# Optimization experiments

Measured on AMD Instinct MI355X. Metric: run time of the kernel, lower is better.

The kernel has to match this reference:

```python
import jax, jax.numpy as jnp
import numpy as np

_MAX_SQRT_GRADIENT = 1000.0

@jax.custom_vjp
def sqrt_bound(x):
    return jnp.sqrt(x)

def _sb_fwd(x):
    return jnp.sqrt(x), x

def _sb_bwd(x, g):
    return (g / jnp.sqrt(jnp.maximum(4.0 * x, 1.0 / (_MAX_SQRT_GRADIENT ** 2))),)

sqrt_bound.defvjp(_sb_fwd, _sb_bwd)


def setup_inputs() -> dict:
    B, S, H, L, NH, K = 2, 4096, 2048, 2048, 16, 4
    BW = L // NH
    key = jax.random.key(0)
    ks = jax.random.split(key, 8)
    f = lambda k, shape: jax.random.normal(k, shape, dtype=jnp.float32) * 0.02
    return {
        "input_states": jax.random.normal(ks[0], (B, S, H), dtype=jnp.float32),
        "Wy": f(ks[1], (H, L)), "by": jnp.zeros((L,), jnp.float32),
        "Wx": f(ks[2], (H, L)), "bx": jnp.zeros((L,), jnp.float32),
        "conv_w": f(ks[3], (L, 1, K)), "conv_b": jnp.zeros((L,), jnp.float32),
        "rec_param": f(ks[4], (L,)),
        "igw": f(ks[5], (NH, BW, BW)), "igb": jnp.zeros((NH, BW), jnp.float32),
        "rgw": f(ks[6], (NH, BW, BW)), "rgb": jnp.zeros((NH, BW), jnp.float32),
        "Wout": f(ks[7], (L, H)), "bout": jnp.zeros((H,), jnp.float32),
        "position_ids": jnp.tile(jnp.arange(S, dtype=jnp.int32), (B, 1)),
    }


def reference(input_states, Wy, by, Wx, bx, conv_w, conv_b, rec_param,
              igw, igb, rgw, rgb, Wout, bout, position_ids):
    B, S, H = input_states.shape
    L = Wy.shape[1]
    NH, BW = igw.shape[0], igw.shape[1]
    K = conv_w.shape[-1]

    # y branch: linear + gelu
    y = jax.nn.gelu(input_states @ Wy + by)                      # [B,S,L]

    # x branch: linear + causal depthwise conv1d
    x = input_states @ Wx + bx                                    # [B,S,L]
    xc = jnp.transpose(x, (0, 2, 1))                              # [B,L,S]
    xc = jax.lax.conv_general_dilated(
        xc, conv_w, window_strides=(1,), padding=[(K - 1, 0)],
        dimension_numbers=("NCH", "OIH", "NCH"), feature_group_count=L)
    x = jnp.transpose(xc, (0, 2, 1)) + conv_b                     # [B,S,L]

    # RG-LRU block-diagonal gates
    xh = x.reshape(B, S, NH, BW)
    ig = jax.nn.sigmoid(jnp.einsum("bsnd,nde->bsne", xh, igw) + igb).reshape(B, S, L)
    rg = jax.nn.sigmoid(jnp.einsum("bsnd,nde->bsne", xh, rgw) + rgb).reshape(B, S, L)

    log_a = -8.0 * rg * jax.nn.softplus(rec_param)                # [B,S,L]
    a = jnp.exp(log_a)
    reset = (position_ids == 0)[:, :, None]                       # [B,S,1]

    mult = sqrt_bound(1.0 - jnp.exp(2.0 * log_a))
    mult = jnp.where(reset, 1.0, mult)
    normed = x * ig * mult                                        # [B,S,L]
    a_eff = jnp.where(reset, 0.0, a)                              # [B,S,L]

    def step(h, inp):
        a_t, x_t = inp
        h = a_t.astype(jnp.float32) * h + x_t.astype(jnp.float32)
        return h, h

    h0 = jnp.zeros((B, L), jnp.float32)
    _, hs = jax.lax.scan(step, h0,
                         (jnp.swapaxes(a_eff, 0, 1), jnp.swapaxes(normed, 0, 1)))
    hs = jnp.swapaxes(hs, 0, 1).astype(input_states.dtype)        # [B,S,L]

    return (hs * y) @ Wout + bout                                 # [B,S,H]
```

## Files before the change

kernel.cpp:

```cpp
#include <hip/hip_runtime.h>
#include <cstdint>
#include <cstddef>

#define B_  2
#define S_  4096
#define H_  2048
#define L_  2048
#define NH_ 16
#define M_  (B_*S_)
#define NC_ 64
#define CS_ 64

typedef unsigned short u16;
typedef short  bf8v  __attribute__((ext_vector_type(8)));
typedef u16    u16x8 __attribute__((ext_vector_type(8)));
typedef float  f32x4 __attribute__((ext_vector_type(4)));

__device__ __forceinline__ float bf2f(u16 u){
  union { unsigned i; float f; } v; v.i = ((unsigned)u) << 16; return v.f;
}
__device__ __forceinline__ u16 f2bf(float f){
  union { float f; unsigned i; } v; v.f = f;
  unsigned u = v.i;
  return (u16)((u + 0x7FFFu + ((u >> 16) & 1u)) >> 16);
}
__device__ __forceinline__ float bfr(float f){ return bf2f(f2bf(f)); }
__device__ __forceinline__ void gld16(const void* g, void* l){
  __builtin_amdgcn_global_load_lds((const __attribute__((address_space(1))) void*)g,
                                   (__attribute__((address_space(3))) void*)l, 16, 0, 0);
}

__global__ __launch_bounds__(256)
void gemm_bf16(const u16* __restrict__ A, int lda,
               const u16* __restrict__ Bt, int K,
               const float* __restrict__ bias1, const float* __restrict__ bias2,
               void* __restrict__ C1, u16* __restrict__ C2, int ldc,
               int gelu_flag, int f32out)
{
  __shared__ u16 Alds[128*64];
  __shared__ u16 Blds[128*64];
  const int t    = threadIdx.x;
  const int lane = t & 63;
  const int w    = t >> 6;
  const int wr   = w >> 1, wc = w & 1;
  const int lr   = lane & 15, lk = lane >> 4;

  const int nwg = gridDim.x * gridDim.y;
  const int bid = blockIdx.y * gridDim.x + blockIdx.x;
  const int cpx = nwg >> 3;
  const int swz = (bid & 7) * cpx + (bid >> 3);
  const int bx  = swz % gridDim.x;
  const int by  = swz / gridDim.x;

  const long rowA0 = (long)by * 128;
  const long colB0 = (long)bx * 128;
  const u16* Ag = A  + rowA0 * lda;
  const u16* Bg = Bt + colB0 * K;
  const int srow = t >> 3, scol = t & 7;

#define STAGE(KT) do {                                                     \
    _Pragma("unroll")                                                      \
    for (int it = 0; it < 4; ++it) {                                       \
      int r  = it*32 + srow;                                               \
      int ca = (scol ^ (r & 7)) * 8;                                       \
      gld16(Ag + (long)r*lda + (long)(KT)*64 + ca, Alds + it*2048 + t*8);  \
      gld16(Bg + (long)r*K   + (long)(KT)*64 + ca, Blds + it*2048 + t*8);  \
    } } while(0)

  f32x4 acc[4][4];
#pragma unroll
  for (int m=0;m<4;m++)
#pragma unroll
    for (int n=0;n<4;n++) acc[m][n] = (f32x4){0.f,0.f,0.f,0.f};

  const int nk = K / 64;
  STAGE(0);
  __syncthreads();

  for (int kt = 0; kt < nk; ++kt) {
    bf8v af[4][2], bv[4][2];
#pragma unroll
    for (int m=0;m<4;m++)
#pragma unroll
      for (int ks=0;ks<2;ks++){
        int r  = wr*64 + m*16 + lr;
        int kb = (ks*32 + lk*8)*2;
        af[m][ks] = *(const bf8v*)((const char*)Alds + r*128 + (kb ^ ((r&7)<<4)));
      }
#pragma unroll
    for (int n=0;n<4;n++)
#pragma unroll
      for (int ks=0;ks<2;ks++){
        int r  = wc*64 + n*16 + lr;
        int kb = (ks*32 + lk*8)*2;
        bv[n][ks] = *(const bf8v*)((const char*)Blds + r*128 + (kb ^ ((r&7)<<4)));
      }
    __syncthreads();
    if (kt + 1 < nk) STAGE(kt + 1);
    __builtin_amdgcn_sched_barrier(0);
#pragma unroll
    for (int ks=0;ks<2;ks++)
#pragma unroll
      for (int m=0;m<4;m++)
#pragma unroll
        for (int n=0;n<4;n++)
          acc[m][n] = __builtin_amdgcn_mfma_f32_16x16x32_bf16(af[m][ks], bv[n][ks], acc[m][n], 0, 0, 0);
    if (kt + 1 < nk) __syncthreads();
  }
#undef STAGE

  u16*   Cb = (u16*)C1;
  float* Cf = (float*)C1;
#pragma unroll
  for (int m=0;m<4;m++){
    long row = rowA0 + wr*64 + m*16 + lk*4;
#pragma unroll
    for (int n=0;n<4;n++){
      int col = (int)colB0 + wc*64 + n*16 + lr;
      bool sec = (C2 != nullptr) && (col >= L_);
      float bvv = sec ? bias2[col - L_] : bias1[col];
      bool gel = gelu_flag && !sec;
#pragma unroll
      for (int rr=0; rr<4; ++rr){
        float v = acc[m][n][rr] + bvv;
        if (gel) {
          float u  = 0.7978845608028654f * (v + 0.044715f * v*v*v);
          float tu = fminf(fmaxf(2.f*u, -80.f), 80.f);
          float e  = __expf(tu);
          float th = (e - 1.f) / (e + 1.f);
          v = 0.5f * v * (1.f + th);
        }
        if (sec)          C2[(row+rr)*(long)L_ + (col - L_)] = f2bf(v);
        else if (f32out)  Cf[(row+rr)*(long)ldc + col] = v;
        else              Cb[(row+rr)*(long)ldc + col] = f2bf(v);
      }
    }
  }
}

__global__ __launch_bounds__(256)
void gates_fused(const u16* __restrict__ Xlin, const float* __restrict__ cw,
                 const float* __restrict__ cb, const u16* __restrict__ Gt,
                 const float* __restrict__ gbias, const float* __restrict__ c8,
                 const int* __restrict__ pos,
                 u16* __restrict__ Ae, u16* __restrict__ Nr,
                 float* __restrict__ Ach, float* __restrict__ Hch)
{
  __shared__ __align__(16) char sm[16384 + 32768];
  const int t  = threadIdx.x;
  const int sc = blockIdx.x;
  const int n  = blockIdx.y;
  const int b  = blockIdx.z;
  const int s0 = sc*64;
  const long rowg0 = (long)b*S_ + s0;

  char* xc = sm;
  u16*  xs = (u16*)(sm + 16384);
  char* bs = sm + 16384;

  for (int it=0; it<5; ++it){
    int slot = it*256 + t;
    if (slot < 67*16){
      int i = slot >> 4, c = slot & 15;
      int s = s0 - 3 + i;
      u16x8 v = (u16x8){0,0,0,0,0,0,0,0};
      if (s >= 0)
        v = *(const u16x8*)(Xlin + ((long)b*S_ + s)*L_ + n*128 + c*8);
      *(u16x8*)(xs + i*128 + c*8) = v;
    }
  }
  __syncthreads();

#pragma unroll
  for (int it=0; it<4; ++it){
    int slot = it*256 + t;
    int row = slot >> 4, c = slot & 15;
    int d0 = c*8;
    float a8[8];
#pragma unroll
    for (int j=0;j<8;j++) a8[j] = cb[n*128 + d0 + j];
#pragma unroll
    for (int k=0;k<4;k++){
      u16x8 xv = *(const u16x8*)(xs + (row+k)*128 + d0);
#pragma unroll
      for (int j=0;j<8;j++)
        a8[j] += bf2f(xv[j]) * cw[(n*128 + d0 + j)*4 + k];
    }
    u16x8 o;
#pragma unroll
    for (int j=0;j<8;j++) o[j] = f2bf(a8[j]);
    *(u16x8*)(xc + row*256 + ((d0*2) ^ ((row&7)<<4))) = o;
  }
  __syncthreads();

  const int w  = t >> 6;
  const int lane = t & 63;
  const int lr = lane & 15, lk = lane >> 4;
  const int arow = w*16 + lr;

  bf8v af[4];
#pragma unroll
  for (int ks=0;ks<4;ks++)
    af[ks] = *(const bf8v*)(xc + arow*256 + ((ks*64 + lk*16) ^ ((arow&7)<<4)));

  f32x4 aig[8], brg[8];
#pragma unroll
  for (int half=0; half<2; ++half){
#pragma unroll
    for (int it=0; it<8; ++it){
      int slot = it*256 + t;
      int jr = slot >> 4, c = slot & 15;
      gld16(Gt + (size_t)(n*256 + half*128 + jr)*128 + (size_t)((c ^ (jr&7))*8),
            bs + slot*16);
    }
    __syncthreads();
#pragma unroll
    for (int nf=0; nf<8; ++nf){
      f32x4 acc = (f32x4){0.f,0.f,0.f,0.f};
      int jrow = nf*16 + lr;
#pragma unroll
      for (int ks=0;ks<4;ks++){
        bf8v bv = *(const bf8v*)(bs + jrow*256 + ((ks*64 + lk*16) ^ ((jrow&7)<<4)));
        acc = __builtin_amdgcn_mfma_f32_16x16x32_bf16(af[ks], bv, acc, 0, 0, 0);
      }
      if (half==0) aig[nf] = acc; else brg[nf] = acc;
    }
    __syncthreads();
  }

  float* wsA = (float*)bs;
  float* wsh = (float*)(bs + 2048);
  bool rst[4];
#pragma unroll
  for (int rr=0; rr<4; ++rr) rst[rr] = (pos[rowg0 + w*16 + lk*4 + rr] == 0);

#pragma unroll
  for (int nf=0; nf<8; ++nf){
    int dl = nf*16 + lr;
    float gb1 = gbias[n*256 + dl];
    float gb2 = gbias[n*256 + 128 + dl];
    float cc8 = c8[n*128 + dl];
    float Aseg = 1.f, hseg = 0.f;
#pragma unroll
    for (int rr=0; rr<4; ++rr){
      int row = w*16 + lk*4 + rr;
      long gs = rowg0 + row;
      float ig = 1.f / (1.f + __expf(-(aig[nf][rr] + gb1)));
      float rg = 1.f / (1.f + __expf(-(brg[nf][rr] + gb2)));
      float la = cc8 * rg;
      float a  = __expf(la);
      float mult = rst[rr] ? 1.f : sqrtf(fmaxf(1.f - __expf(2.f*la), 0.f));
      u16 xv = *(const u16*)(xc + row*256 + ((dl*2) ^ ((row&7)<<4)));
      float x = bf2f(xv);
      float nrv = bfr(x * ig * mult);
      float aev = rst[rr] ? 0.f : bfr(a);
      Nr[gs*L_ + n*128 + dl] = f2bf(nrv);
      Ae[gs*L_ + n*128 + dl] = f2bf(aev);
      hseg = fmaf(aev, hseg, nrv);
      Aseg *= aev;
    }
    {
      float Ap = __shfl_xor(Aseg, 16);
      float hp = __shfl_xor(hseg, 16);
      bool low = ((lk & 1) == 0);
      float Alo = low ? Aseg : Ap, Ahi = low ? Ap : Aseg;
      float hlo = low ? hseg : hp, hhi = low ? hp : hseg;
      Aseg = Alo * Ahi; hseg = fmaf(Ahi, hlo, hhi);
      Ap = __shfl_xor(Aseg, 32);
      hp = __shfl_xor(hseg, 32);
      low = ((lk & 2) == 0);
      Alo = low ? Aseg : Ap; Ahi = low ? Ap : Aseg;
      hlo = low ? hseg : hp; hhi = low ? hp : hseg;
      Aseg = Alo * Ahi; hseg = fmaf(Ahi, hlo, hhi);
    }
    if (lk == 0){ wsA[w*128 + dl] = Aseg; wsh[w*128 + dl] = hseg; }
  }
  __syncthreads();
  if (t < 128){
    float A = wsA[t], h = wsh[t];
#pragma unroll
    for (int ww=1; ww<4; ++ww){
      float Aw = wsA[ww*128 + t], hw = wsh[ww*128 + t];
      h = fmaf(Aw, h, hw);
      A *= Aw;
    }
    long o = ((long)b*NC_ + sc)*L_ + n*128 + t;
    Ach[o] = A; Hch[o] = h;
  }
}

__global__ __launch_bounds__(256)
void prep_all(const float* __restrict__ Wy, const float* __restrict__ Wx,
              const float* __restrict__ Wout,
              u16* __restrict__ WyT, u16* __restrict__ WxT, u16* __restrict__ WoT,
              const float* __restrict__ igw, const float* __restrict__ rgw,
              const float* __restrict__ igb, const float* __restrict__ rgb,
              const float* __restrict__ rec, u16* __restrict__ Gt,
              float* __restrict__ gbias, float* __restrict__ c8,
              const float* __restrict__ X, u16* __restrict__ Xb)
{
  const int bidg = blockIdx.x;
  const int t = threadIdx.x;
  if (bidg < 3072) {
    int z   = bidg >> 10;
    int rem = bidg & 1023;
    const float* in  = (z == 0) ? Wy  : (z == 1) ? Wx  : Wout;
    u16*         out = (z == 0) ? WyT : (z == 1) ? WxT : WoT;
    const int R = 2048, C = 2048;
    __shared__ float tile[64][65];
    int tc = (rem & 31) * 64, tr = (rem >> 5) * 64;
    int r  = t >> 2, c0 = (t & 3) * 16;
#pragma unroll
    for (int i=0;i<4;i++)
      *(f32x4*)(&tile[r][c0 + i*4]) = *(const f32x4*)(in + (long)(tr+r)*C + tc + c0 + i*4);
    __syncthreads();
    int nl = t >> 2;
#pragma unroll
    for (int it=0; it<2; ++it){
      int g = (t & 3) + it*4;
      u16x8 o;
#pragma unroll
      for (int e=0;e<8;e++) o[e] = f2bf(tile[g*8+e][nl]);
      *(u16x8*)(out + (long)(tc+nl)*R + tr + g*8) = o;
    }
  } else if (bidg < 5120) {
    int idx = (bidg - 3072)*256 + t;
    int d = idx & 127, g = idx >> 7;
    int n = g >> 8, j = g & 255;
    float v = (j < 128) ? igw[(n*128 + d)*128 + j] : rgw[(n*128 + d)*128 + (j-128)];
    Gt[idx] = f2bf(v);
    if (idx < NH_*256) {
      int nn = idx >> 8, jj = idx & 255;
      gbias[idx] = (jj < 128) ? igb[nn*128 + jj] : rgb[nn*128 + jj - 128];
    }
    if (idx < L_) c8[idx] = -8.f * log1pf(__expf(rec[idx]));
  } else {
    long idx = (long)(bidg - 5120)*256 + t;
    f32x4 a = *(const f32x4*)(X + idx*8);
    f32x4 b = *(const f32x4*)(X + idx*8 + 4);
    u16x8 o;
#pragma unroll
    for (int e=0;e<4;e++){ o[e] = f2bf(a[e]); o[4+e] = f2bf(b[e]); }
    *(u16x8*)(Xb + idx*8) = o;
  }
}

__global__ __launch_bounds__(256)
void scan3(const u16* __restrict__ Ae, const u16* __restrict__ Nr,
           const float* __restrict__ Ach, const float* __restrict__ Hch,
           const u16* __restrict__ Y, u16* __restrict__ Z)
{
  int t = threadIdx.x;
  int l = (blockIdx.x & 7)*256 + t;
  int c = (NC_-1) - ((blockIdx.x >> 3) & (NC_-1));
  int b = blockIdx.x >> 9;
  float h = 0.f;
#pragma unroll 4
  for (int cc = 0; cc < c; ++cc){
    long o = ((long)b*NC_ + cc)*L_ + l;
    h = fmaf(Ach[o], h, Hch[o]);
  }
  long base = ((long)b*S_ + (long)c*CS_)*L_ + l;
#pragma unroll 8
  for (int s=0; s<CS_; ++s){
    long o = base + (long)s*L_;
    h = fmaf(bf2f(Ae[o]), h, bf2f(Nr[o]));
    Z[o] = f2bf(h * bf2f(Y[o]));
  }
}

extern "C" void kernel_launch(void* const* d_in, const int* in_sizes, int n_in,
                              void* d_out, int out_size, void* d_ws, size_t ws_size,
                              hipStream_t stream)
{
  (void)in_sizes; (void)n_in; (void)out_size; (void)ws_size;
  const float* X    = (const float*)d_in[0];
  const float* Wy   = (const float*)d_in[1];
  const float* by   = (const float*)d_in[2];
  const float* Wx   = (const float*)d_in[3];
  const float* bx   = (const float*)d_in[4];
  const float* cw   = (const float*)d_in[5];
  const float* cb   = (const float*)d_in[6];
  const float* rec  = (const float*)d_in[7];
  const float* igw  = (const float*)d_in[8];
  const float* igb  = (const float*)d_in[9];
  const float* rgw  = (const float*)d_in[10];
  const float* rgb  = (const float*)d_in[11];
  const float* Wout = (const float*)d_in[12];
  const float* bout = (const float*)d_in[13];
  const int*   pos  = (const int*)d_in[14];
  float* out = (float*)d_out;

  char* ws = (char*)d_ws;
  size_t o_Xbf  = 0;
  size_t o_Xlin = o_Xbf  + (size_t)M_*H_*2;
  size_t o_WyT  = o_Xlin + (size_t)M_*L_*2;
  size_t o_WxT  = o_WyT  + (size_t)H_*L_*2;
  size_t o_WoT  = o_WxT  + (size_t)H_*L_*2;
  size_t o_Gt   = o_WoT  + (size_t)L_*H_*2;
  size_t o_gb   = o_Gt   + (size_t)NH_*256*128*2;
  size_t o_c8   = o_gb   + 4096*4;
  size_t o_Y    = o_c8   + 2048*4;
  size_t o_xc   = o_Y    + (size_t)M_*L_*2;
  size_t o_Ae   = o_xc   + (size_t)M_*L_*2;
  size_t o_Nr   = o_Ae   + (size_t)M_*L_*2;
  size_t o_Ach  = o_Nr   + (size_t)M_*L_*2;
  size_t o_Hch  = o_Ach  + (size_t)B_*NC_*L_*4;

  u16*   Xbf   = (u16*)(ws + o_Xbf);
  u16*   Xlin  = (u16*)(ws + o_Xlin);
  u16*   WyT   = (u16*)(ws + o_WyT);
  u16*   WxT   = (u16*)(ws + o_WxT);
  u16*   WoT   = (u16*)(ws + o_WoT);
  u16*   Gt    = (u16*)(ws + o_Gt);
  float* gbias = (float*)(ws + o_gb);
  float* c8    = (float*)(ws + o_c8);
  u16*   Y     = (u16*)(ws + o_Y);
  u16*   Z     = (u16*)(ws + o_xc);
  u16*   Ae    = (u16*)(ws + o_Ae);
  u16*   Nr    = (u16*)(ws + o_Nr);
  float* Ach   = (float*)(ws + o_Ach);
  float* Hch   = (float*)(ws + o_Hch);

  dim3 blk(256);
  prep_all<<<dim3(13312), blk, 0, stream>>>(Wy, Wx, Wout, WyT, WxT, WoT,
                                            igw, rgw, igb, rgb, rec, Gt, gbias, c8,
                                            X, Xbf);
  gemm_bf16<<<dim3(32,64), blk, 0, stream>>>(Xbf, H_, WyT, H_, by, bx, Y, Xlin, L_, 1, 0);
  gates_fused<<<dim3(NC_, NH_, B_), blk, 0, stream>>>(Xlin, cw, cb, Gt, gbias, c8, pos,
                                                      Ae, Nr, Ach, Hch);
  scan3<<<dim3(1024), blk, 0, stream>>>(Ae, Nr, Ach, Hch, Y, Z);
  gemm_bf16<<<dim3(16,64), blk, 0, stream>>>(Z, L_, WoT, L_, bout, bout, out, nullptr, H_, 0, 1);
}
```

Baseline: 412.6 us.

## Replace GEMM with 256x256 tile, 8-wave, double-buffered ping-pong pipelined kernel

Replaces the 128x128 single-buffered bf16 GEMM with a 256x256-tile, 512-thread kernel. It uses double-buffered LDS (128KB), inline-asm ds_read_b128 with immediate offsets, and explicit waitcnt and barrier phases so that global-to-LDS loads and LDS reads overlap MFMA work. s_setprio is raised around the MFMA blocks. The larger tile increases data reuse per LDS byte, at the cost of fewer workgroups (512 and 256 blocks) and higher register and LDS pressure, which may hurt occupancy. Tile wraparound with modulo loads redundant tiles in the last iterations.

```diff
diff --git a/kernel.cpp b/kernel.cpp
--- a/kernel.cpp
+++ b/kernel.cpp
@@ -29,20 +29,99 @@
   __builtin_amdgcn_global_load_lds((const __attribute__((address_space(1))) void*)g,
                                    (__attribute__((address_space(3))) void*)l, 16, 0, 0);
 }
-
-__global__ __launch_bounds__(256)
-void gemm_bf16(const u16* __restrict__ A, int lda,
-               const u16* __restrict__ Bt, int K,
-               const float* __restrict__ bias1, const float* __restrict__ bias2,
-               void* __restrict__ C1, u16* __restrict__ C2, int ldc,
-               int gelu_flag, int f32out)
+__device__ __forceinline__ unsigned ldsoff(const void* p){
+  return (unsigned)(uintptr_t)(const __attribute__((address_space(3))) void*)p;
+}
+template<int IMM>
+__device__ __forceinline__ bf8v dsr(unsigned addr){
+  bf8v r;
+  asm volatile("ds_read_b128 %0, %1 offset:%c2" : "=v"(r) : "v"(addr), "i"(IMM));
+  return r;
+}
+
+#define SB0_()     __builtin_amdgcn_sched_barrier(0)
+#define BARRIER_() do{ __builtin_amdgcn_s_barrier(); SB0_(); }while(0)
+#define LGKM0_()   do{ asm volatile("s_waitcnt lgkmcnt(0)" ::: "memory"); SB0_(); }while(0)
+#define VMC8_()    do{ asm volatile("s_waitcnt vmcnt(8)" ::: "memory"); SB0_(); }while(0)
+
+struct StageCtx { const u16* sA; const u16* sB; int lda; int K; char* ldsc; unsigned dst; };
+
+__device__ __forceinline__ void stgA(const StageCtx& c, int buf, int h, int tile){
+#pragma unroll
+  for (int r=0;r<2;r++){
+    int rr = h*128 + r*64;
+    gld16(c.sA + (size_t)rr*c.lda + (size_t)tile*64, c.ldsc + buf*32768 + c.dst + rr*128);
+  }
+}
+__device__ __forceinline__ void stgB(const StageCtx& c, int buf, int h, int tile){
+#pragma unroll
+  for (int r=0;r<2;r++){
+    int rr = h*128 + r*64;
+    gld16(c.sB + (size_t)rr*c.K + (size_t)tile*64, c.ldsc + 65536 + buf*32768 + c.dst + rr*128);
+  }
+}
+
+#define MFMAQ(ARR, MH, NHH) do{                                                 \
+  __builtin_amdgcn_s_setprio(1);                                                \
+  _Pragma("unroll") for (int ks=0;ks<2;ks++)                                    \
+  _Pragma("unroll") for (int dm=0;dm<4;dm++)                                    \
+  _Pragma("unroll") for (int dn=0;dn<2;dn++)                                    \
+    acc[(MH)*4+dm][(NHH)*2+dn] = __builtin_amdgcn_mfma_f32_16x16x32_bf16(       \
+        ARR[dm][ks], b[(NHH)*2+dn][ks], acc[(MH)*4+dm][(NHH)*2+dn], 0,0,0);     \
+  __builtin_amdgcn_s_setprio(0);                                                \
+}while(0)
+
+template<int D>
+__device__ __forceinline__ void tile_phase(
+    bf8v (&a)[4][2], bf8v (&aN)[4][2], bf8v (&b)[4][2], f32x4 (&acc)[8][4],
+    unsigned aA0, unsigned aA1, unsigned aB0, unsigned aB1,
+    const StageCtx& ctx, int tp2)
 {
-  __shared__ u16 Alds[128*64];
-  __shared__ u16 Blds[128*64];
+  constexpr int DB = D*32768;
+  constexpr int OB = (1-D)*32768;
+  b[2][0]=dsr<DB+4096>(aB0); b[2][1]=dsr<DB+4096>(aB1);
+  b[3][0]=dsr<DB+6144>(aB0); b[3][1]=dsr<DB+6144>(aB1);
+  SB0_();
+  MFMAQ(a, 0, 0);
+  LGKM0_(); BARRIER_();
+  aN[0][0]=dsr<DB+ 8192>(aA0); aN[0][1]=dsr<DB+ 8192>(aA1);
+  aN[1][0]=dsr<DB+10240>(aA0); aN[1][1]=dsr<DB+10240>(aA1);
+  aN[2][0]=dsr<DB+12288>(aA0); aN[2][1]=dsr<DB+12288>(aA1);
+  aN[3][0]=dsr<DB+14336>(aA0); aN[3][1]=dsr<DB+14336>(aA1);
+  SB0_();
+  MFMAQ(a, 0, 1);
+  LGKM0_(); BARRIER_();
+  stgB(ctx, D, 0, tp2);
+  SB0_();
+  MFMAQ(aN, 1, 0);
+  SB0_();
+  stgB(ctx, D, 1, tp2);
+  stgA(ctx, D, 0, tp2);
+  stgA(ctx, D, 1, tp2);
+  VMC8_();
+  a[0][0]=dsr<OB+   0>(aA0); a[0][1]=dsr<OB+   0>(aA1);
+  a[1][0]=dsr<OB+2048>(aA0); a[1][1]=dsr<OB+2048>(aA1);
+  a[2][0]=dsr<OB+4096>(aA0); a[2][1]=dsr<OB+4096>(aA1);
+  a[3][0]=dsr<OB+6144>(aA0); a[3][1]=dsr<OB+6144>(aA1);
+  b[0][0]=dsr<OB+   0>(aB0); b[0][1]=dsr<OB+   0>(aB1);
+  b[1][0]=dsr<OB+2048>(aB0); b[1][1]=dsr<OB+2048>(aB1);
+  SB0_();
+  MFMAQ(aN, 1, 1);
+  LGKM0_(); BARRIER_();
+}
+
+__global__ __launch_bounds__(512)
+void gemm256p(const u16* __restrict__ A, int lda,
+              const u16* __restrict__ Bt, int K,
+              const float* __restrict__ bias1, const float* __restrict__ bias2,
+              void* __restrict__ C1, u16* __restrict__ C2, int ldc,
+              int gelu_flag, int f32out)
+{
+  __shared__ __align__(16) u16 lds[65536];
   const int t    = threadIdx.x;
   const int lane = t & 63;
   const int w    = t >> 6;
-  const int wr   = w >> 1, wc = w & 1;
+  const int wm   = w >> 2, wn = w & 3;
   const int lr   = lane & 15, lk = lane >> 4;
 
   const int nwg = gridDim.x * gridDim.y;
@@ -52,77 +131,69 @@
   const int bx  = swz % gridDim.x;
   const int by  = swz / gridDim.x;
 
-  const long rowA0 = (long)by * 128;
-  const long colB0 = (long)bx * 128;
+  const long rowA0 = (long)by * 256;
+  const long colB0 = (long)bx * 256;
   const u16* Ag = A  + rowA0 * lda;
   const u16* Bg = Bt + colB0 * K;
-  const int srow = t >> 3, scol = t & 7;
-
-#define STAGE(KT) do {                                                     \
-    _Pragma("unroll")                                                      \
-    for (int it = 0; it < 4; ++it) {                                       \
-      int r  = it*32 + srow;                                               \
-      int ca = (scol ^ (r & 7)) * 8;                                       \
-      gld16(Ag + (long)r*lda + (long)(KT)*64 + ca, Alds + it*2048 + t*8);  \
-      gld16(Bg + (long)r*K   + (long)(KT)*64 + ca, Blds + it*2048 + t*8);  \
-    } } while(0)
-
-  f32x4 acc[4][4];
-#pragma unroll
-  for (int m=0;m<4;m++)
+
+  char* ldsc = (char*)lds;
+  StageCtx ctx;
+  ctx.sA  = Ag + (size_t)(t>>3)*lda + ((t&7) ^ ((t>>3)&7))*8;
+  ctx.sB  = Bg + (size_t)(t>>3)*K   + ((t&7) ^ ((t>>3)&7))*8;
+  ctx.lda = lda; ctx.K = K; ctx.ldsc = ldsc;
+  ctx.dst = (unsigned)((t>>3)*128 + (t&7)*16);
+
+  const unsigned lb  = ldsoff(lds);
+  const unsigned swx = (unsigned)((lr & 7) << 4);
+  const unsigned aA0 = lb + (wm*128 + lr)*128 + ((      lk*16) ^ swx);
+  const unsigned aA1 = lb + (wm*128 + lr)*128 + ((64 +  lk*16) ^ swx);
+  const unsigned aB0 = lb + 65536 + (wn*64 + lr)*128 + ((      lk*16) ^ swx);
+  const unsigned aB1 = lb + 65536 + (wn*64 + lr)*128 + ((64 +  lk*16) ^ swx);
+
+  f32x4 acc[8][4];
+#pragma unroll
+  for (int m=0;m<8;m++)
 #pragma unroll
     for (int n=0;n<4;n++) acc[m][n] = (f32x4){0.f,0.f,0.f,0.f};
-
-  const int nk = K / 64;
-  STAGE(0);
-  __syncthreads();
-
-  for (int kt = 0; kt < nk; ++kt) {
-    bf8v af[4][2], bv[4][2];
-#pragma unroll
-    for (int m=0;m<4;m++)
-#pragma unroll
-      for (int ks=0;ks<2;ks++){
-        int r  = wr*64 + m*16 + lr;
-        int kb = (ks*32 + lk*8)*2;
-        af[m][ks] = *(const bf8v*)((const char*)Alds + r*128 + (kb ^ ((r&7)<<4)));
-      }
-#pragma unroll
-    for (int n=0;n<4;n++)
-#pragma unroll
-      for (int ks=0;ks<2;ks++){
-        int r  = wc*64 + n*16 + lr;
-        int kb = (ks*32 + lk*8)*2;
-        bv[n][ks] = *(const bf8v*)((const char*)Blds + r*128 + (kb ^ ((r&7)<<4)));
-      }
-    __syncthreads();
-    if (kt + 1 < nk) STAGE(kt + 1);
-    __builtin_amdgcn_sched_barrier(0);
-#pragma unroll
-    for (int ks=0;ks<2;ks++)
-#pragma unroll
-      for (int m=0;m<4;m++)
-#pragma unroll
-        for (int n=0;n<4;n++)
-          acc[m][n] = __builtin_amdgcn_mfma_f32_16x16x32_bf16(af[m][ks], bv[n][ks], acc[m][n], 0, 0, 0);
-    if (kt + 1 < nk) __syncthreads();
-  }
-#undef STAGE
+  bf8v a[4][2], aN[4][2], b[4][2];
+
+  const int nkt = K / 64;
+  stgB(ctx, 0, 0, 0);        stgB(ctx, 0, 1, 0);
+  stgA(ctx, 0, 0, 0);        stgA(ctx, 0, 1, 0);
+  stgB(ctx, 1, 0, 1 % nkt);  stgB(ctx, 1, 1, 1 % nkt);
+  stgA(ctx, 1, 0, 1 % nkt);  stgA(ctx, 1, 1, 1 % nkt);
+  VMC8_();
+  BARRIER_();
+  a[0][0]=dsr<   0>(aA0); a[0][1]=dsr<   0>(aA1);
+  a[1][0]=dsr<2048>(aA0); a[1][1]=dsr<2048>(aA1);
+  a[2][0]=dsr<4096>(aA0); a[2][1]=dsr<4096>(aA1);
+  a[3][0]=dsr<6144>(aA0); a[3][1]=dsr<6144>(aA1);
+  b[0][0]=dsr<   0>(aB0); b[0][1]=dsr<   0>(aB1);
+  b[1][0]=dsr<2048>(aB0); b[1][1]=dsr<2048>(aB1);
+  LGKM0_();
+
+  for (int i = 0; i < nkt/2; ++i) {
+    int t0 = 2*i;
+    tile_phase<0>(a, aN, b, acc, aA0, aA1, aB0, aB1, ctx, (t0+2)%nkt);
+    tile_phase<1>(a, aN, b, acc, aA0, aA1, aB0, aB1, ctx, (t0+3)%nkt);
+  }
 
   u16*   Cb = (u16*)C1;
   float* Cf = (float*)C1;
-#pragma unroll
-  for (int m=0;m<4;m++){
-    long row = rowA0 + wr*64 + m*16 + lk*4;
-#pragma unroll
-    for (int n=0;n<4;n++){
-      int col = (int)colB0 + wc*64 + n*16 + lr;
+  const long rowW = rowA0 + wm*128;
+  const int  colW = (int)colB0 + wn*64;
+#pragma unroll
+  for (int mf=0;mf<8;mf++){
+    long row = rowW + mf*16 + lk*4;
+#pragma unroll
+    for (int nf=0;nf<4;nf++){
+      int col = colW + nf*16 + lr;
       bool sec = (C2 != nullptr) && (col >= L_);
       float bvv = sec ? bias2[col - L_] : bias1[col];
       bool gel = gelu_flag && !sec;
 #pragma unroll
       for (int rr=0; rr<4; ++rr){
-        float v = acc[m][n][rr] + bvv;
+        float v = acc[mf][nf][rr] + bvv;
         if (gel) {
           float u  = 0.7978845608028654f * (v + 0.044715f * v*v*v);
           float tu = fminf(fmaxf(2.f*u, -80.f), 80.f);
@@ -426,9 +497,9 @@
   prep_all<<<dim3(13312), blk, 0, stream>>>(Wy, Wx, Wout, WyT, WxT, WoT,
                                             igw, rgw, igb, rgb, rec, Gt, gbias, c8,
                                             X, Xbf);
-  gemm_bf16<<<dim3(32,64), blk, 0, stream>>>(Xbf, H_, WyT, H_, by, bx, Y, Xlin, L_, 1, 0);
+  gemm256p<<<dim3(16,32), dim3(512), 0, stream>>>(Xbf, H_, WyT, H_, by, bx, Y, Xlin, L_, 1, 0);
   gates_fused<<<dim3(NC_, NH_, B_), blk, 0, stream>>>(Xlin, cw, cb, Gt, gbias, c8, pos,
                                                       Ae, Nr, Ach, Hch);
   scan3<<<dim3(1024), blk, 0, stream>>>(Ae, Nr, Ach, Hch, Y, Z);
-  gemm_bf16<<<dim3(16,64), blk, 0, stream>>>(Z, L_, WoT, L_, bout, bout, out, nullptr, H_, 0, 1);
-}
+  gemm256p<<<dim3(8,32), dim3(512), 0, stream>>>(Z, L_, WoT, L_, bout, bout, out, nullptr, H_, 0, 1);
+}
```

Result: slower. 516.1 us (+25.1%).
